# Optimization experiments

Hardware: AMD Instinct MI355X
Metric: run time of the kernel (lower is better)

## Reference

```python
import jax, jax.numpy as jnp
import numpy as np
import math

N, V, NH = 4096, 256, 64  # samples, variables (channels), hidden units


def _permutation_skeleton(v):
    # perm[c] is a (V, V-1) selection matrix keeping all variables j != c,
    # columns ordered by j (faithful to CustomizedRelaModule.permutation_matrix
    # with skeleton = 1 - I, so max_dim = V - 1 and no zero-padding remains).
    perm = np.zeros((v, v, v - 1), dtype=np.float32)
    for c in range(v):
        idx = np.delete(np.arange(v), c)
        perm[c, idx, np.arange(v - 1)] = 1.0
    return jnp.asarray(perm)


def setup_inputs() -> dict:
    key = jax.random.key(0)
    k = jax.random.split(key, 7)
    data = jax.random.normal(k[0], (N, V), dtype=jnp.float32)
    adj = jax.random.normal(k[1], (V, V), dtype=jnp.float32)        # self.adj_matrix ~ N(0,1)
    neurons = jax.random.normal(k[2], (NH, V), dtype=jnp.float32)   # self.neurons ~ N(0,1)
    s1 = 1.0 / math.sqrt(V - 1)  # input_layer: uniform(-1/sqrt(in), 1/sqrt(in)), in = max_dim = V-1
    w_in = jax.random.uniform(k[3], (V, V - 1, NH), minval=-s1, maxval=s1, dtype=jnp.float32)
    b_in = jax.random.uniform(k[4], (V, NH), minval=-s1, maxval=s1, dtype=jnp.float32)
    s2 = 1.0 / math.sqrt(NH)
    w_out = jax.random.uniform(k[5], (V, NH, 1), minval=-s2, maxval=s2, dtype=jnp.float32)
    b_out = jax.random.uniform(k[6], (V, 1), minval=-s2, maxval=s2, dtype=jnp.float32)
    perm = _permutation_skeleton(V)
    return {"data": data, "adj": adj, "neurons": neurons,
            "w_in": w_in, "b_in": b_in, "w_out": w_out, "b_out": b_out,
            "perm": perm}


def reference(data, adj, neurons, w_in, b_in, w_out, b_out, perm):
    # categorical_matrix is identity, so the adjacency passed is adj itself.
    # Linear3D input layer with adj + permutation:
    #   masked[n, c, k] = sum_j data[n, j] * adj[j, c] * perm[c, j, k]
    # i.e. per channel c, gather adj-weighted inputs for all j != c.
    masked = jnp.einsum('nj,jc,cjk->nck', data, adj, perm)  # (N, V, V-1)
    # per-channel linear + tanh
    h = jnp.tanh(jnp.einsum('nck,ckh->nch', masked, w_in) + b_in[None])  # (N, V, NH)
    # output Linear3D with adj_matrix = neurons (NH, V): elementwise gate then per-channel linear
    gated = h * neurons.T[None]  # (N, V, NH)
    out = jnp.einsum('nch,cho->nco', gated, w_out) + b_out[None]  # (N, V, 1)
    return (adj, out[..., 0])
```

## Files before the change

### kernel.cpp

```cpp
#include <hip/hip_runtime.h>
#include <hip/hip_bf16.h>

#define NS   4096
#define NV   256
#define NHID 64
#define K2F  2.8853900817779268f

typedef short s8v __attribute__((ext_vector_type(8)));
typedef float f4v __attribute__((ext_vector_type(4)));

typedef __attribute__((address_space(1))) const unsigned int GU;
typedef __attribute__((address_space(3))) unsigned int LU;

__device__ __forceinline__ void gload16(const void* gp, void* lp) {
    __builtin_amdgcn_global_load_lds((GU*)gp, (LU*)lp, 16, 0, 0);
}

__device__ __forceinline__ unsigned short f2bf(float x) {
    __hip_bfloat16 h = __float2bfloat16(x);
    return *reinterpret_cast<unsigned short*>(&h);
}

__global__ __launch_bounds__(256) void k_prep_all(
        const float* __restrict__ adj, const float* __restrict__ w_in,
        unsigned short* __restrict__ W2t,
        const float* __restrict__ data, unsigned short* __restrict__ dataB,
        float* __restrict__ out0,
        const float* __restrict__ neurons, const float* __restrict__ w_out,
        const float* __restrict__ b_out, float* __restrict__ g2, float* __restrict__ BO,
        const float* __restrict__ b_in, float* __restrict__ bi2)
{
    __shared__ float t[64][65];
    const int blk = blockIdx.x, tid = threadIdx.x;
    if (blk < 1024) {
        int c  = blk >> 2;
        int k0 = (blk & 3) * 64;
#pragma unroll
        for (int i = 0; i < 16; ++i) {
            int lin = i * 256 + tid;
            int kr = lin >> 6, h = lin & 63;
            int k = k0 + kr;
            float v = 0.0f;
            if (k != c) {
                int m = k - (k > c ? 1 : 0);
                v = adj[k * NV + c] * w_in[((size_t)c * 255 + m) * 64 + h];
            }
            t[kr][h] = v;
        }
        __syncthreads();
#pragma unroll
        for (int i = 0; i < 16; ++i) {
            int lin = i * 256 + tid;
            int h = lin >> 6, kr = lin & 63;
            W2t[((size_t)(c * 64 + h)) * NV + k0 + kr] = f2bf(t[kr][h]);
        }
        return;
    }
    const int b = blk - 1024;
    if (b < 1024) {
        int i = b * 256 + tid;
        float4 v = reinterpret_cast<const float4*>(data)[i];
        ushort4 o = make_ushort4(f2bf(v.x), f2bf(v.y), f2bf(v.z), f2bf(v.w));
        reinterpret_cast<ushort4*>(dataB)[i] = o;
    } else if (b < 1088) {
        int i = (b - 1024) * 256 + tid;
        reinterpret_cast<float4*>(out0)[i] = reinterpret_cast<const float4*>(adj)[i];
    } else if (b < 1152) {
        int j = (b - 1088) * 256 + tid;
        int c = j >> 6, h = j & 63;
        float gv = neurons[h * NV + c] * w_out[j];
        g2[j] = 2.0f * gv;
        float s = gv;
        s += __shfl_xor(s, 1);  s += __shfl_xor(s, 2);  s += __shfl_xor(s, 4);
        s += __shfl_xor(s, 8);  s += __shfl_xor(s, 16); s += __shfl_xor(s, 32);
        if ((tid & 63) == 0) BO[c] = b_out[c] + s;
    } else {
        int i = (b - 1152) * 256 + tid;
        float4 v = reinterpret_cast<const float4*>(b_in)[i];
        v.x *= K2F; v.y *= K2F; v.z *= K2F; v.w *= K2F;
        reinterpret_cast<float4*>(bi2)[i] = v;
    }
}

__global__ __launch_bounds__(256, 3) void k_gemm_fused(
        const unsigned short* __restrict__ dataB,
        const unsigned short* __restrict__ W2t,
        const float* __restrict__ g2,
        const float* __restrict__ bi2,
        const float* __restrict__ BO,
        float* __restrict__ out1)
{
    __shared__ __align__(16) char lds[65536];
    const int tid  = threadIdx.x;
    const int w    = tid >> 6;
    const int lane = tid & 63;
    const int lq   = lane >> 4, lr = lane & 15;
    const int wr   = w >> 1, wc = w & 1;

    const int orig = (int)blockIdx.x;
    const int swz  = (orig & 7) * 512 + (orig >> 3);
    const int bm0  = (swz & 31) << 7;
    const int bn0  = (swz >> 5) << 7;

    f4v acc[4][4];
#pragma unroll
    for (int mi = 0; mi < 4; ++mi)
#pragma unroll
        for (int ni = 0; ni < 4; ++ni)
            acc[mi][ni] = (f4v){0.f, 0.f, 0.f, 0.f};

    unsigned int offA[4], offB[4], ldso[4];
#pragma unroll
    for (int t = 0; t < 4; ++t) {
        int o = w * 4096 + t * 1024 + lane * 16;
        int row = o >> 7;
        int inner = (o & 127) ^ ((row & 7) << 4);
        ldso[t] = (unsigned)(w * 4096 + t * 1024);
        offA[t] = (unsigned)(bm0 + row) * 512u + (unsigned)inner;
        offB[t] = (unsigned)(bn0 + row) * 512u + (unsigned)inner;
    }

    const char* dA = (const char*)dataB;
    const char* dB = (const char*)W2t;

#define STAGE(KT, BUFO)                                                        \
    do {                                                                       \
        _Pragma("unroll")                                                      \
        for (int t = 0; t < 4; ++t)                                            \
            gload16(dA + (size_t)offA[t] + (KT) * 128, lds + (BUFO) + ldso[t]); \
        _Pragma("unroll")                                                      \
        for (int t = 0; t < 4; ++t)                                            \
            gload16(dB + (size_t)offB[t] + (KT) * 128, lds + (BUFO) + 16384 + ldso[t]); \
    } while (0)

    STAGE(0, 0);
    STAGE(1, 32768);

#pragma unroll
    for (int kt = 0; kt < 4; ++kt) {
        const int bufo = (kt & 1) << 15;
        if (kt < 3) { asm volatile("s_waitcnt vmcnt(8)" ::: "memory"); }
        else        { asm volatile("s_waitcnt vmcnt(0)" ::: "memory"); }
        __builtin_amdgcn_sched_barrier(0);
        __builtin_amdgcn_s_barrier();
        __builtin_amdgcn_sched_barrier(0);

#pragma unroll
        for (int kk = 0; kk < 2; ++kk) {
            s8v afr[4], bfr[4];
#pragma unroll
            for (int mi = 0; mi < 4; ++mi) {
                int ml = wr * 64 + mi * 16 + lr;
                int inner = (kk * 64 + (lq << 4)) ^ ((ml & 7) << 4);
                afr[mi] = *reinterpret_cast<const s8v*>(lds + bufo + ml * 128 + inner);
            }
#pragma unroll
            for (int ni = 0; ni < 4; ++ni) {
                int nl = wc * 64 + ni * 16 + lr;
                int inner = (kk * 64 + (lq << 4)) ^ ((nl & 7) << 4);
                bfr[ni] = *reinterpret_cast<const s8v*>(lds + bufo + 16384 + nl * 128 + inner);
            }
            __builtin_amdgcn_s_setprio(1);
#pragma unroll
            for (int mi = 0; mi < 4; ++mi)
#pragma unroll
                for (int ni = 0; ni < 4; ++ni)
                    acc[mi][ni] = __builtin_amdgcn_mfma_f32_16x16x32_bf16(
                        bfr[ni], afr[mi], acc[mi][ni], 0, 0, 0);
            __builtin_amdgcn_s_setprio(0);
        }

        __builtin_amdgcn_sched_barrier(0);
        __builtin_amdgcn_s_barrier();
        __builtin_amdgcn_sched_barrier(0);
        if (kt < 2) STAGE(kt + 2, bufo);
    }
#undef STAGE

    const int cidx = (bn0 >> 6) + wc;
    float4 g2v[4], bi2v[4];
#pragma unroll
    for (int ni = 0; ni < 4; ++ni) {
        int base = cidx * 64 + ni * 16 + lq * 4;
        g2v[ni]  = *(const float4*)&g2 [base];
        bi2v[ni] = *(const float4*)&bi2[base];
    }
    const float BOv = BO[cidx];

    float s0, s1, s2, s3;
#define EPI_TERM(T, GC, BC, RR)                                                \
    { float mm = __builtin_fmaf(acc[mi][ni][RR], K2F, (BC));                   \
      float e  = __builtin_amdgcn_exp2f(mm);                                   \
      (T) = __builtin_fmaf((GC), __builtin_amdgcn_rcpf(e + 1.0f), (T)); }
#define EPI_MI(T)                                                              \
    { float t = 0.f;                                                           \
      _Pragma("unroll")                                                        \
      for (int ni = 0; ni < 4; ++ni) {                                         \
          EPI_TERM(t, g2v[ni].x, bi2v[ni].x, 0);                               \
          EPI_TERM(t, g2v[ni].y, bi2v[ni].y, 1);                               \
          EPI_TERM(t, g2v[ni].z, bi2v[ni].z, 2);                               \
          EPI_TERM(t, g2v[ni].w, bi2v[ni].w, 3);                               \
      }                                                                        \
      t += __shfl_xor(t, 16);                                                  \
      t += __shfl_xor(t, 32);                                                  \
      (T) = t; }
    { const int mi = 0; EPI_MI(s0); }
    { const int mi = 1; EPI_MI(s1); }
    { const int mi = 2; EPI_MI(s2); }
    { const int mi = 3; EPI_MI(s3); }
#undef EPI_MI
#undef EPI_TERM
    float v = lane < 16 ? s0 : (lane < 32 ? s1 : (lane < 48 ? s2 : s3));
    out1[(unsigned)(bm0 + wr * 64 + lane) * NV + cidx] = BOv - v;
}

extern "C" void kernel_launch(void* const* d_in, const int* in_sizes, int n_in,
                              void* d_out, int out_size, void* d_ws, size_t ws_size,
                              hipStream_t stream) {
    const float* data    = (const float*)d_in[0];
    const float* adj     = (const float*)d_in[1];
    const float* neurons = (const float*)d_in[2];
    const float* w_in    = (const float*)d_in[3];
    const float* b_in    = (const float*)d_in[4];
    const float* w_out   = (const float*)d_in[5];
    const float* b_out   = (const float*)d_in[6];

    float* out0 = (float*)d_out;
    float* out1 = out0 + NV * NV;

    unsigned short* dataB = (unsigned short*)d_ws;
    unsigned short* W2t   = (unsigned short*)((char*)d_ws + 2097152);
    float*          g2    = (float*)((char*)d_ws + 10485760);
    float*          bi2   = (float*)((char*)d_ws + 10551296);
    float*          BO    = (float*)((char*)d_ws + 10616832);

    hipLaunchKernelGGL(k_prep_all, dim3(2192), dim3(256), 0, stream,
                       adj, w_in, W2t, data, dataB, out0,
                       neurons, w_out, b_out, g2, BO, b_in, bi2);
    hipLaunchKernelGGL(k_gemm_fused, dim3(4096), dim3(256), 0, stream,
                       dataB, W2t, g2, bi2, BO, out1);
}
```

Before: 62.78 us.

## Load B operand directly into registers and halve LDS double buffer

The W2t (B) tile no longer goes through LDS. Each wave now reads its own 64-column B fragments from global memory straight into registers one k-step ahead, and only the A tile stays in a 32 KB LDS double buffer. The prefetch depth for A drops from two stages to one, and the vmcnt waits are changed to match. This removes the LDS writes and reads for B and cuts LDS use, which could allow more blocks per CU. In exchange, B is read twice from global (by both wave rows), uses more registers, and global latency is less hidden.

```diff
diff --git a/kernel.cpp b/kernel.cpp
--- a/kernel.cpp
+++ b/kernel.cpp
@@ -90,7 +90,7 @@
         const float* __restrict__ BO,
         float* __restrict__ out1)
 {
-    __shared__ __align__(16) char lds[65536];
+    __shared__ __align__(16) char lds[32768];
     const int tid  = threadIdx.x;
     const int w    = tid >> 6;
     const int lane = tid & 63;
@@ -109,7 +109,7 @@
         for (int ni = 0; ni < 4; ++ni)
             acc[mi][ni] = (f4v){0.f, 0.f, 0.f, 0.f};
 
-    unsigned int offA[4], offB[4], ldso[4];
+    unsigned int offA[4], ldso[4];
 #pragma unroll
     for (int t = 0; t < 4; ++t) {
         int o = w * 4096 + t * 1024 + lane * 16;
@@ -117,29 +117,42 @@
         int inner = (o & 127) ^ ((row & 7) << 4);
         ldso[t] = (unsigned)(w * 4096 + t * 1024);
         offA[t] = (unsigned)(bm0 + row) * 512u + (unsigned)inner;
-        offB[t] = (unsigned)(bn0 + row) * 512u + (unsigned)inner;
-    }
-
+    }
     const char* dA = (const char*)dataB;
     const char* dB = (const char*)W2t;
 
-#define STAGE(KT, BUFO)                                                        \
+    const char* pB[4];
+#pragma unroll
+    for (int ni = 0; ni < 4; ++ni)
+        pB[ni] = dB + (size_t)(bn0 + wc * 64 + ni * 16 + lr) * 512 + lq * 16;
+
+    s8v BW[8];
+
+#define STAGE_A(KT, BUFO)                                                      \
     do {                                                                       \
         _Pragma("unroll")                                                      \
         for (int t = 0; t < 4; ++t)                                            \
             gload16(dA + (size_t)offA[t] + (KT) * 128, lds + (BUFO) + ldso[t]); \
+    } while (0)
+
+#define LOADB(KT)                                                              \
+    do {                                                                       \
         _Pragma("unroll")                                                      \
-        for (int t = 0; t < 4; ++t)                                            \
-            gload16(dB + (size_t)offB[t] + (KT) * 128, lds + (BUFO) + 16384 + ldso[t]); \
+        for (int ni = 0; ni < 4; ++ni) {                                       \
+            BW[ni]     = *reinterpret_cast<const s8v*>(pB[ni] + (KT) * 128);   \
+            BW[4 + ni] = *reinterpret_cast<const s8v*>(pB[ni] + (KT) * 128 + 64); \
+        }                                                                      \
     } while (0)
 
-    STAGE(0, 0);
-    STAGE(1, 32768);
+    STAGE_A(0, 0);
+    LOADB(0);
 
 #pragma unroll
     for (int kt = 0; kt < 4; ++kt) {
-        const int bufo = (kt & 1) << 15;
-        if (kt < 3) { asm volatile("s_waitcnt vmcnt(8)" ::: "memory"); }
+        const int bufo = (kt & 1) << 14;
+        if (kt < 3) STAGE_A(kt + 1, bufo ^ 16384);
+        __builtin_amdgcn_sched_barrier(0);
+        if (kt < 3) { asm volatile("s_waitcnt vmcnt(4)" ::: "memory"); }
         else        { asm volatile("s_waitcnt vmcnt(0)" ::: "memory"); }
         __builtin_amdgcn_sched_barrier(0);
         __builtin_amdgcn_s_barrier();
@@ -147,35 +160,31 @@
 
 #pragma unroll
         for (int kk = 0; kk < 2; ++kk) {
-            s8v afr[4], bfr[4];
+            s8v afr[4];
 #pragma unroll
             for (int mi = 0; mi < 4; ++mi) {
                 int ml = wr * 64 + mi * 16 + lr;
                 int inner = (kk * 64 + (lq << 4)) ^ ((ml & 7) << 4);
                 afr[mi] = *reinterpret_cast<const s8v*>(lds + bufo + ml * 128 + inner);
             }
-#pragma unroll
-            for (int ni = 0; ni < 4; ++ni) {
-                int nl = wc * 64 + ni * 16 + lr;
-                int inner = (kk * 64 + (lq << 4)) ^ ((nl & 7) << 4);
-                bfr[ni] = *reinterpret_cast<const s8v*>(lds + bufo + 16384 + nl * 128 + inner);
-            }
             __builtin_amdgcn_s_setprio(1);
 #pragma unroll
             for (int mi = 0; mi < 4; ++mi)
 #pragma unroll
                 for (int ni = 0; ni < 4; ++ni)
                     acc[mi][ni] = __builtin_amdgcn_mfma_f32_16x16x32_bf16(
-                        bfr[ni], afr[mi], acc[mi][ni], 0, 0, 0);
+                        BW[kk * 4 + ni], afr[mi], acc[mi][ni], 0, 0, 0);
             __builtin_amdgcn_s_setprio(0);
         }
 
+        if (kt < 3) LOADB(kt + 1);
+
         __builtin_amdgcn_sched_barrier(0);
         __builtin_amdgcn_s_barrier();
         __builtin_amdgcn_sched_barrier(0);
-        if (kt < 2) STAGE(kt + 2, bufo);
-    }
-#undef STAGE
+    }
+#undef STAGE_A
+#undef LOADB
 
     const int cidx = (bn0 >> 6) + wc;
     float4 g2v[4], bi2v[4];
```

After: 91.80 us. 46.2% more time.

## Make GEMM persistent over N tiles with 32x32 MFMA and cross-tile prefetch

Applied to the files above, without the earlier changes.

The fused GEMM moves from one block per 128x128 output tile (4096 blocks) to 512 blocks, each looping over 8 consecutive N tiles for a fixed 128-row M strip. The K-loop pipeline continues across tile boundaries, so the next tile's first K stage is prefetched during the current tile's last stage. The MFMA shape changes from 16x16x32 to 32x32x16, with a reworked epilogue and a 2-block occupancy hint. The goals are to cut launch and block-startup overhead, hide load latency between tiles, and reduce LDS fragment reads per MFMA. In exchange there is less parallelism (512 blocks) and the tanh epilogue now runs serially between tiles.

```diff
diff --git a/kernel.cpp b/kernel.cpp
--- a/kernel.cpp
+++ b/kernel.cpp
@@ -7,7 +7,7 @@
 #define K2F  2.8853900817779268f
 
 typedef short s8v __attribute__((ext_vector_type(8)));
-typedef float f4v __attribute__((ext_vector_type(4)));
+typedef float f16v __attribute__((ext_vector_type(16)));
 
 typedef __attribute__((address_space(1))) const unsigned int GU;
 typedef __attribute__((address_space(3))) unsigned int LU;
@@ -82,7 +82,7 @@
     }
 }
 
-__global__ __launch_bounds__(256, 3) void k_gemm_fused(
+__global__ __launch_bounds__(256, 2) void k_gemm_fused(
         const unsigned short* __restrict__ dataB,
         const unsigned short* __restrict__ W2t,
         const float* __restrict__ g2,
@@ -94,124 +94,136 @@
     const int tid  = threadIdx.x;
     const int w    = tid >> 6;
     const int lane = tid & 63;
-    const int lq   = lane >> 4, lr = lane & 15;
-    const int wr   = w >> 1, wc = w & 1;
-
-    const int orig = (int)blockIdx.x;
-    const int swz  = (orig & 7) * 512 + (orig >> 3);
-    const int bm0  = (swz & 31) << 7;
-    const int bn0  = (swz >> 5) << 7;
-
-    f4v acc[4][4];
-#pragma unroll
-    for (int mi = 0; mi < 4; ++mi)
-#pragma unroll
-        for (int ni = 0; ni < 4; ++ni)
-            acc[mi][ni] = (f4v){0.f, 0.f, 0.f, 0.f};
-
-    unsigned int offA[4], offB[4], ldso[4];
-#pragma unroll
-    for (int t = 0; t < 4; ++t) {
-        int o = w * 4096 + t * 1024 + lane * 16;
-        int row = o >> 7;
-        int inner = (o & 127) ^ ((row & 7) << 4);
-        ldso[t] = (unsigned)(w * 4096 + t * 1024);
-        offA[t] = (unsigned)(bm0 + row) * 512u + (unsigned)inner;
-        offB[t] = (unsigned)(bn0 + row) * 512u + (unsigned)inner;
-    }
+    const int l31  = lane & 31;
+    const int hi   = lane >> 5;
+    const int wm   = w & 1, wn = w >> 1;
+
+    const int bid    = (int)blockIdx.x;
+    const int nchunk = (bid & 7) * 2 + ((bid >> 3) & 1);
+    const int mstrip = bid >> 4;
+    const int m0     = mstrip * 128;
+
+    f16v acc[2][2];
+#pragma unroll
+    for (int mi = 0; mi < 2; ++mi)
+#pragma unroll
+        for (int ni = 0; ni < 2; ++ni)
+            acc[mi][ni] = (f16v)(0.0f);
 
     const char* dA = (const char*)dataB;
     const char* dB = (const char*)W2t;
-
-#define STAGE(KT, BUFO)                                                        \
+    unsigned rowL[4], innL[4];
+#pragma unroll
+    for (int l = 0; l < 4; ++l) {
+        int o = l * 4096 + tid * 16;
+        rowL[l] = (unsigned)(o >> 7);
+        innL[l] = (unsigned)((o & 127) ^ (((o >> 7) & 7) << 4));
+    }
+    const unsigned t16 = (unsigned)tid * 16;
+
+#define STAGE(KT, NB, BUFO)                                                    \
     do {                                                                       \
         _Pragma("unroll")                                                      \
-        for (int t = 0; t < 4; ++t)                                            \
-            gload16(dA + (size_t)offA[t] + (KT) * 128, lds + (BUFO) + ldso[t]); \
+        for (int l = 0; l < 4; ++l)                                            \
+            gload16(dA + (size_t)(m0 + rowL[l]) * 512 + (KT) * 128 + innL[l],  \
+                    lds + (BUFO) + l * 4096 + t16);                            \
         _Pragma("unroll")                                                      \
-        for (int t = 0; t < 4; ++t)                                            \
-            gload16(dB + (size_t)offB[t] + (KT) * 128, lds + (BUFO) + 16384 + ldso[t]); \
+        for (int l = 0; l < 4; ++l)                                            \
+            gload16(dB + (size_t)((NB) + rowL[l]) * 512 + (KT) * 128 + innL[l],\
+                    lds + (BUFO) + 16384 + l * 4096 + t16);                    \
     } while (0)
 
-    STAGE(0, 0);
-    STAGE(1, 32768);
-
-#pragma unroll
-    for (int kt = 0; kt < 4; ++kt) {
-        const int bufo = (kt & 1) << 15;
-        if (kt < 3) { asm volatile("s_waitcnt vmcnt(8)" ::: "memory"); }
-        else        { asm volatile("s_waitcnt vmcnt(0)" ::: "memory"); }
-        __builtin_amdgcn_sched_barrier(0);
-        __builtin_amdgcn_s_barrier();
-        __builtin_amdgcn_sched_barrier(0);
-
-#pragma unroll
-        for (int kk = 0; kk < 2; ++kk) {
-            s8v afr[4], bfr[4];
-#pragma unroll
-            for (int mi = 0; mi < 4; ++mi) {
-                int ml = wr * 64 + mi * 16 + lr;
-                int inner = (kk * 64 + (lq << 4)) ^ ((ml & 7) << 4);
-                afr[mi] = *reinterpret_cast<const s8v*>(lds + bufo + ml * 128 + inner);
+    STAGE(0, nchunk * 1024, 0);
+
+    for (int nt = 0; nt < 8; ++nt) {
+        const int ntile = nchunk * 8 + nt;
+        const int nb    = ntile * 128;
+        const int nbN   = nb + 128;
+
+#pragma unroll
+        for (int kt = 0; kt < 4; ++kt) {
+            const int bufo = (kt & 1) << 15;
+            if (kt < 3)            STAGE(kt + 1, nb, bufo ^ 32768);
+            else if (nt < 7)       STAGE(0, nbN, bufo ^ 32768);
+            __builtin_amdgcn_sched_barrier(0);
+            if (kt == 3 && nt == 7) { asm volatile("s_waitcnt vmcnt(0)" ::: "memory"); }
+            else                    { asm volatile("s_waitcnt vmcnt(8)" ::: "memory"); }
+            __builtin_amdgcn_sched_barrier(0);
+            __builtin_amdgcn_s_barrier();
+            __builtin_amdgcn_sched_barrier(0);
+
+#pragma unroll
+            for (int kk = 0; kk < 4; ++kk) {
+                const int inB = kk * 32 + hi * 16;
+                s8v afr[2], bfr[2];
+#pragma unroll
+                for (int mi = 0; mi < 2; ++mi) {
+                    int ml = wm * 64 + mi * 32 + l31;
+                    afr[mi] = *reinterpret_cast<const s8v*>(
+                        lds + bufo + ml * 128 + (inB ^ ((ml & 7) << 4)));
+                }
+#pragma unroll
+                for (int ni = 0; ni < 2; ++ni) {
+                    int nl = wn * 64 + ni * 32 + l31;
+                    bfr[ni] = *reinterpret_cast<const s8v*>(
+                        lds + bufo + 16384 + nl * 128 + (inB ^ ((nl & 7) << 4)));
+                }
+                __builtin_amdgcn_s_setprio(1);
+#pragma unroll
+                for (int mi = 0; mi < 2; ++mi)
+#pragma unroll
+                    for (int ni = 0; ni < 2; ++ni)
+                        acc[mi][ni] = __builtin_amdgcn_mfma_f32_32x32x16_bf16(
+                            bfr[ni], afr[mi], acc[mi][ni], 0, 0, 0);
+                __builtin_amdgcn_s_setprio(0);
             }
-#pragma unroll
-            for (int ni = 0; ni < 4; ++ni) {
-                int nl = wc * 64 + ni * 16 + lr;
-                int inner = (kk * 64 + (lq << 4)) ^ ((nl & 7) << 4);
-                bfr[ni] = *reinterpret_cast<const s8v*>(lds + bufo + 16384 + nl * 128 + inner);
+
+            __builtin_amdgcn_sched_barrier(0);
+            __builtin_amdgcn_s_barrier();
+            __builtin_amdgcn_sched_barrier(0);
+        }
+
+        const int cidx = ntile * 2 + wn;
+        const float BOv = BO[cidx];
+        float s0 = 0.f, s1 = 0.f;
+#pragma unroll
+        for (int ni = 0; ni < 2; ++ni) {
+#pragma unroll
+            for (int q = 0; q < 4; ++q) {
+                int base = cidx * 64 + ni * 32 + q * 8 + hi * 4;
+                float4 gq = *(const float4*)&g2 [base];
+                float4 bq = *(const float4*)&bi2[base];
+#pragma unroll
+                for (int j = 0; j < 4; ++j) {
+                    const int r = q * 4 + j;
+                    float gj = j == 0 ? gq.x : (j == 1 ? gq.y : (j == 2 ? gq.z : gq.w));
+                    float bj = j == 0 ? bq.x : (j == 1 ? bq.y : (j == 2 ? bq.z : bq.w));
+                    {
+                        float mm = __builtin_fmaf(acc[0][ni][r], K2F, bj);
+                        float e  = __builtin_amdgcn_exp2f(mm);
+                        s0 = __builtin_fmaf(gj, __builtin_amdgcn_rcpf(e + 1.0f), s0);
+                    }
+                    {
+                        float mm = __builtin_fmaf(acc[1][ni][r], K2F, bj);
+                        float e  = __builtin_amdgcn_exp2f(mm);
+                        s1 = __builtin_fmaf(gj, __builtin_amdgcn_rcpf(e + 1.0f), s1);
+                    }
+                }
             }
-            __builtin_amdgcn_s_setprio(1);
-#pragma unroll
-            for (int mi = 0; mi < 4; ++mi)
-#pragma unroll
-                for (int ni = 0; ni < 4; ++ni)
-                    acc[mi][ni] = __builtin_amdgcn_mfma_f32_16x16x32_bf16(
-                        bfr[ni], afr[mi], acc[mi][ni], 0, 0, 0);
-            __builtin_amdgcn_s_setprio(0);
-        }
-
-        __builtin_amdgcn_sched_barrier(0);
-        __builtin_amdgcn_s_barrier();
-        __builtin_amdgcn_sched_barrier(0);
-        if (kt < 2) STAGE(kt + 2, bufo);
+        }
+        s0 += __shfl_xor(s0, 32);
+        s1 += __shfl_xor(s1, 32);
+        if (lane < 32) {
+            out1[(unsigned)(m0 + wm * 64 + l31) * NV + cidx]      = BOv - s0;
+            out1[(unsigned)(m0 + wm * 64 + 32 + l31) * NV + cidx] = BOv - s1;
+        }
+#pragma unroll
+        for (int mi = 0; mi < 2; ++mi)
+#pragma unroll
+            for (int ni = 0; ni < 2; ++ni)
+                acc[mi][ni] = (f16v)(0.0f);
     }
 #undef STAGE
-
-    const int cidx = (bn0 >> 6) + wc;
-    float4 g2v[4], bi2v[4];
-#pragma unroll
-    for (int ni = 0; ni < 4; ++ni) {
-        int base = cidx * 64 + ni * 16 + lq * 4;
-        g2v[ni]  = *(const float4*)&g2 [base];
-        bi2v[ni] = *(const float4*)&bi2[base];
-    }
-    const float BOv = BO[cidx];
-
-    float s0, s1, s2, s3;
-#define EPI_TERM(T, GC, BC, RR)                                                \
-    { float mm = __builtin_fmaf(acc[mi][ni][RR], K2F, (BC));                   \
-      float e  = __builtin_amdgcn_exp2f(mm);                                   \
-      (T) = __builtin_fmaf((GC), __builtin_amdgcn_rcpf(e + 1.0f), (T)); }
-#define EPI_MI(T)                                                              \
-    { float t = 0.f;                                                           \
-      _Pragma("unroll")                                                        \
-      for (int ni = 0; ni < 4; ++ni) {                                         \
-          EPI_TERM(t, g2v[ni].x, bi2v[ni].x, 0);                               \
-          EPI_TERM(t, g2v[ni].y, bi2v[ni].y, 1);                               \
-          EPI_TERM(t, g2v[ni].z, bi2v[ni].z, 2);                               \
-          EPI_TERM(t, g2v[ni].w, bi2v[ni].w, 3);                               \
-      }                                                                        \
-      t += __shfl_xor(t, 16);                                                  \
-      t += __shfl_xor(t, 32);                                                  \
-      (T) = t; }
-    { const int mi = 0; EPI_MI(s0); }
-    { const int mi = 1; EPI_MI(s1); }
-    { const int mi = 2; EPI_MI(s2); }
-    { const int mi = 3; EPI_MI(s3); }
-#undef EPI_MI
-#undef EPI_TERM
-    float v = lane < 16 ? s0 : (lane < 32 ? s1 : (lane < 48 ? s2 : s3));
-    out1[(unsigned)(bm0 + wr * 64 + lane) * NV + cidx] = BOv - v;
 }
 
 extern "C" void kernel_launch(void* const* d_in, const int* in_sizes, int n_in,
@@ -237,6 +249,6 @@
     hipLaunchKernelGGL(k_prep_all, dim3(2192), dim3(256), 0, stream,
                        adj, w_in, W2t, data, dataB, out0,
                        neurons, w_out, b_out, g2, BO, b_in, bi2);
-    hipLaunchKernelGGL(k_gemm_fused, dim3(4096), dim3(256), 0, stream,
+    hipLaunchKernelGGL(k_gemm_fused, dim3(512), dim3(256), 0, stream,
                        dataB, W2t, g2, bi2, BO, out1);
 }
```

Result: slower. 64.81 us (+3.2%).
